# Performance work log

Hardware: AMD Instinct MI355X
Metric: run time of the kernel (lower is better)

The kernel has to match this reference:

```python
import jax, jax.numpy as jnp
import numpy as np

N_NODES = 100000
N_EDGES = 3200000
D_FEAT = 256
HIDDEN = 16


def setup_inputs() -> dict:
    key = jax.random.key(0)
    k1, k2, k3, k4 = jax.random.split(key, 4)
    x = jax.random.normal(k1, (N_NODES, D_FEAT), dtype=jnp.float32)
    edge_index = jax.random.randint(k2, (2, N_EDGES), 0, N_NODES, dtype=jnp.int64)
    # GCNConv linear weight (Glorot-ish scale) and bias
    W = jax.random.normal(k3, (D_FEAT, HIDDEN), dtype=jnp.float32) / np.sqrt(D_FEAT)
    b_conv = jnp.zeros((HIDDEN,), dtype=jnp.float32)
    W_fc = jax.random.normal(k4, (HIDDEN, 1), dtype=jnp.float32) / np.sqrt(HIDDEN)
    b_fc = jnp.zeros((1,), dtype=jnp.float32)
    return {"x": x, "edge_index": edge_index, "W": W, "b_conv": b_conv,
            "W_fc": W_fc, "b_fc": b_fc}


def reference(x, edge_index, W, b_conv, W_fc, b_fc):
    N = x.shape[0]
    # --- GCNConv: add self-loops, symmetric normalization, transform, scatter-add ---
    loop = jnp.arange(N, dtype=edge_index.dtype)
    src = jnp.concatenate([edge_index[0], loop])  # message sources (x_j)
    dst = jnp.concatenate([edge_index[1], loop])  # aggregation targets
    # degree of target nodes (edge weights = 1, self-loops included)
    deg = jax.ops.segment_sum(jnp.ones_like(dst, dtype=x.dtype), dst, num_segments=N)
    dinv = jnp.where(deg > 0, jax.lax.rsqrt(deg), 0.0)
    norm = dinv[src] * dinv[dst]  # [E+N]
    h = x @ W                       # [N, hidden] transform before propagation
    msg = h[src] * norm[:, None]    # gather + scale
    agg = jax.ops.segment_sum(msg, dst, num_segments=N)  # scatter-add
    out = agg + b_conv
    return out @ W_fc + b_fc
```

## Files before the change

kernel.cpp:

```cpp
#include <hip/hip_runtime.h>

#define DF 256
#define HID 16
#define WB 512
#define PBITS 8
#define PMAX 512

__global__ void __launch_bounds__(512)
hist_sval_kernel(const float* __restrict__ x, const int* __restrict__ dst,
                 const float* __restrict__ Wm, const float* __restrict__ W_fc,
                 unsigned* __restrict__ cntT, float* __restrict__ sv,
                 int N, int E, int P, int Epw) {
    __shared__ unsigned h[PMAX];
    for (int i = threadIdx.x; i < P; i += blockDim.x) h[i] = 0u;
    __syncthreads();
    const int w = blockIdx.x;
    const size_t e0 = (size_t)w * Epw;
    int m = (int)((size_t)E > e0 ? (size_t)E - e0 : 0);
    if (m > Epw) m = Epw;
    for (int i = threadIdx.x; i < m; i += blockDim.x)
        atomicAdd(&h[((unsigned)dst[e0 + i]) >> PBITS], 1u);
    __syncthreads();
    for (int p = threadIdx.x; p < P; p += blockDim.x)
        cntT[(size_t)p * WB + w] = h[p];

    const int lane = threadIdx.x & 63, wid = threadIdx.x >> 6;
    float a0 = 0.f, a1 = 0.f, a2 = 0.f, a3 = 0.f;
    const float* wrow = Wm + (size_t)(lane * 4) * HID;
#pragma unroll
    for (int j = 0; j < HID; ++j) {
        float f = W_fc[j];
        a0 += wrow[j] * f;
        a1 += wrow[HID + j] * f;
        a2 += wrow[2 * HID + j] * f;
        a3 += wrow[3 * HID + j] * f;
    }
    for (int row = blockIdx.x * 8 + wid; row < N; row += WB * 8) {
        float4 xv = reinterpret_cast<const float4*>(x + (size_t)row * DF)[lane];
        float acc = xv.x * a0 + xv.y * a1 + xv.z * a2 + xv.w * a3;
#pragma unroll
        for (int off = 32; off > 0; off >>= 1) acc += __shfl_xor(acc, off, 64);
        if (lane == 0) sv[row] = acc;
    }
}

__global__ void __launch_bounds__(WB)
rowscan_kernel(unsigned* __restrict__ cntT, unsigned* __restrict__ rowTotal) {
    __shared__ unsigned wsum[8];
    const int p = blockIdx.x, t = threadIdx.x;
    const int lane = t & 63, wid = t >> 6;
    unsigned v = cntT[(size_t)p * WB + t];
    unsigned xi = v;
#pragma unroll
    for (int off = 1; off < 64; off <<= 1) {
        unsigned u = __shfl_up(xi, off, 64);
        if (lane >= off) xi += u;
    }
    if (lane == 63) wsum[wid] = xi;
    __syncthreads();
    if (t < 8) {
        unsigned u = wsum[t];
#pragma unroll
        for (int off = 1; off < 8; off <<= 1) {
            unsigned uu = __shfl_up(u, off, 64);
            if (t >= off) u += uu;
        }
        wsum[t] = u;
    }
    __syncthreads();
    unsigned base = wid ? wsum[wid - 1] : 0u;
    cntT[(size_t)p * WB + t] = xi - v + base;
    if (t == 0) rowTotal[p] = wsum[7];
}

__global__ void __launch_bounds__(PMAX)
partscan_kernel(const unsigned* __restrict__ rowTotal, unsigned* __restrict__ partBase,
                int P, int E) {
    __shared__ unsigned wsum[8];
    const int t = threadIdx.x, lane = t & 63, wid = t >> 6;
    unsigned v = (t < P) ? rowTotal[t] : 0u;
    unsigned xi = v;
#pragma unroll
    for (int off = 1; off < 64; off <<= 1) {
        unsigned u = __shfl_up(xi, off, 64);
        if (lane >= off) xi += u;
    }
    if (lane == 63) wsum[wid] = xi;
    __syncthreads();
    if (t < 8) {
        unsigned u = wsum[t];
#pragma unroll
        for (int off = 1; off < 8; off <<= 1) {
            unsigned uu = __shfl_up(u, off, 64);
            if (t >= off) u += uu;
        }
        wsum[t] = u;
    }
    __syncthreads();
    unsigned base = wid ? wsum[wid - 1] : 0u;
    if (t < P) partBase[t] = xi - v + base;
    if (t == 0) partBase[P] = (unsigned)E;
}

__global__ void __launch_bounds__(512)
binscatter_kernel(const int* __restrict__ src, const int* __restrict__ dst,
                  const unsigned* __restrict__ cntT, const unsigned* __restrict__ partBase,
                  unsigned* __restrict__ sorted, int P, int E, int Epw) {
    __shared__ unsigned cur[PMAX];
    const int w = blockIdx.x;
    for (int p = threadIdx.x; p < P; p += blockDim.x)
        cur[p] = partBase[p] + cntT[(size_t)p * WB + w];
    __syncthreads();
    const size_t e0 = (size_t)w * Epw;
    int m = (int)((size_t)E > e0 ? (size_t)E - e0 : 0);
    if (m > Epw) m = Epw;
    for (int i = threadIdx.x; i < m; i += blockDim.x) {
        unsigned s = (unsigned)src[e0 + i];
        unsigned d = (unsigned)dst[e0 + i];
        unsigned slot = atomicAdd(&cur[d >> PBITS], 1u);
        sorted[slot] = (s << PBITS) | (d & 255u);
    }
}

__global__ void __launch_bounds__(1024)
degfin_kernel(const unsigned* __restrict__ sorted, const unsigned* __restrict__ partBase,
              const float* __restrict__ sv, float* __restrict__ dinv,
              float* __restrict__ tval, int N) {
    __shared__ unsigned dc[256];
    const int p = blockIdx.x;
    if (threadIdx.x < 256) dc[threadIdx.x] = 0u;
    __syncthreads();
    const unsigned b0 = partBase[p], b1 = partBase[p + 1];
    for (unsigned j = b0 + threadIdx.x; j < b1; j += blockDim.x)
        atomicAdd(&dc[sorted[j] & 255u], 1u);
    __syncthreads();
    if (threadIdx.x < 256) {
        int i = (p << PBITS) + (int)threadIdx.x;
        if (i < N) {
            float deg = 1.0f + (float)dc[threadIdx.x];
            float di = rsqrtf(deg);
            dinv[i] = di;
            tval[i] = sv[i] * di;
        }
    }
}

__global__ void __launch_bounds__(1024)
reduce_kernel(const unsigned* __restrict__ sorted, const unsigned* __restrict__ partBase,
              const float* __restrict__ tval, const float* __restrict__ dinv,
              const float* __restrict__ sv, const float* __restrict__ b_conv,
              const float* __restrict__ W_fc, const float* __restrict__ b_fc,
              float* __restrict__ out, int N) {
    __shared__ float facc[256];
    const int p = blockIdx.x;
    if (threadIdx.x < 256) facc[threadIdx.x] = 0.f;
    __syncthreads();
    const unsigned b0 = partBase[p], b1 = partBase[p + 1];
    for (unsigned j = b0 + threadIdx.x; j < b1; j += blockDim.x) {
        unsigned e = sorted[j];
        atomicAdd(&facc[e & 255u], tval[e >> PBITS]);
    }
    __syncthreads();
    if (threadIdx.x < 256) {
        int i = (p << PBITS) + (int)threadIdx.x;
        if (i < N) {
            float c = 0.f;
#pragma unroll
            for (int j = 0; j < HID; ++j) c += b_conv[j] * W_fc[j];
            float di = dinv[i];
            out[i] = sv[i] * di * di + c + b_fc[0] + di * facc[threadIdx.x];
        }
    }
}

__global__ void fb_sval(const float* __restrict__ x, const float* __restrict__ Wm,
                        const float* __restrict__ W_fc, float* __restrict__ sv, int N) {
    __shared__ float wl[DF];
    int k = threadIdx.x;
    float a = 0.f;
#pragma unroll
    for (int j = 0; j < HID; ++j) a += Wm[k * HID + j] * W_fc[j];
    wl[k] = a;
    __syncthreads();
    int lane = threadIdx.x & 63, wid = threadIdx.x >> 6;
    float4 wv = reinterpret_cast<const float4*>(wl)[lane];
    for (int row = blockIdx.x * 4 + wid; row < N; row += gridDim.x * 4) {
        float4 xv = reinterpret_cast<const float4*>(x + (size_t)row * DF)[lane];
        float acc = xv.x * wv.x + xv.y * wv.y + xv.z * wv.z + xv.w * wv.w;
#pragma unroll
        for (int off = 32; off > 0; off >>= 1) acc += __shfl_xor(acc, off, 64);
        if (lane == 0) sv[row] = acc;
    }
}
__global__ void fb_count(const int* __restrict__ dst, unsigned* __restrict__ cnt, int E) {
    int stride = gridDim.x * blockDim.x;
    for (int e = blockIdx.x * blockDim.x + threadIdx.x; e < E; e += stride)
        atomicAdd(&cnt[dst[e]], 1u);
}
__global__ void fb_node(const unsigned* __restrict__ cnt, const float* __restrict__ sv,
                        const float* __restrict__ b_conv, const float* __restrict__ W_fc,
                        const float* __restrict__ b_fc, float* __restrict__ dinv,
                        float* __restrict__ tval, float* __restrict__ out, int N) {
    int i = blockIdx.x * blockDim.x + threadIdx.x;
    if (i < N) {
        float c = 0.f;
#pragma unroll
        for (int j = 0; j < HID; ++j) c += b_conv[j] * W_fc[j];
        float deg = 1.0f + (float)cnt[i];
        float di = rsqrtf(deg);
        float s = sv[i];
        dinv[i] = di; tval[i] = s * di;
        out[i] = s / deg + c + b_fc[0];
    }
}
__global__ void fb_scatter(const int* __restrict__ src, const int* __restrict__ dst,
                           const float* __restrict__ tval, const float* __restrict__ dinv,
                           float* __restrict__ out, int E) {
    int stride = gridDim.x * blockDim.x;
    for (int e = blockIdx.x * blockDim.x + threadIdx.x; e < E; e += stride) {
        int si = src[e], di = dst[e];
        atomicAdd(&out[di], tval[si] * dinv[di]);
    }
}

extern "C" void kernel_launch(void* const* d_in, const int* in_sizes, int n_in,
                              void* d_out, int out_size, void* d_ws, size_t ws_size,
                              hipStream_t stream) {
    const float* x      = (const float*)d_in[0];
    const int*   ei     = (const int*)d_in[1];
    const float* Wm     = (const float*)d_in[2];
    const float* b_conv = (const float*)d_in[3];
    const float* W_fc   = (const float*)d_in[4];
    const float* b_fc   = (const float*)d_in[5];
    float* out = (float*)d_out;

    const int N = in_sizes[0] / DF;
    const int E = in_sizes[1] / 2;
    const int* src = ei;
    const int* dst = ei + E;

    const int P   = (N + 255) >> PBITS;
    const int Epw = (E + WB - 1) / WB;

    char* ws = (char*)d_ws;
    float* sv   = (float*)ws;
    float* dinv = sv + N;
    float* tval = dinv + N;
    unsigned* cntT     = (unsigned*)(tval + N);
    unsigned* rowTotal = cntT + (size_t)P * WB;
    unsigned* partBase = rowTotal + 512;
    unsigned* sorted   = partBase + 520;

    const size_t need = ((size_t)3 * N + (size_t)P * WB + 512 + 520 + (size_t)E) * 4;

    if (P >= 1 && P <= PMAX && N <= (1 << 23) && ws_size >= need) {
        hist_sval_kernel<<<WB, 512, 0, stream>>>(x, dst, Wm, W_fc, cntT, sv, N, E, P, Epw);
        rowscan_kernel<<<P, WB, 0, stream>>>(cntT, rowTotal);
        partscan_kernel<<<1, PMAX, 0, stream>>>(rowTotal, partBase, P, E);
        binscatter_kernel<<<WB, 512, 0, stream>>>(src, dst, cntT, partBase, sorted, P, E, Epw);
        degfin_kernel<<<P, 1024, 0, stream>>>(sorted, partBase, sv, dinv, tval, N);
        reduce_kernel<<<P, 1024, 0, stream>>>(sorted, partBase, tval, dinv, sv,
                                              b_conv, W_fc, b_fc, out, N);
    } else {
        unsigned* fcnt = (unsigned*)(tval + N);
        hipMemsetAsync(fcnt, 0, (size_t)N * 4, stream);
        fb_sval<<<2048, 256, 0, stream>>>(x, Wm, W_fc, sv, N);
        fb_count<<<2048, 256, 0, stream>>>(dst, fcnt, E);
        fb_node<<<(N + 255) / 256, 256, 0, stream>>>(fcnt, sv, b_conv, W_fc, b_fc, dinv, tval, out, N);
        fb_scatter<<<2048, 256, 0, stream>>>(src, dst, tval, dinv, out, E);
    }
}
```

Before: 90.96 us.

## Move x-projection into degree kernel, double histogram blocks, unroll edge loops

The x·(W·W_fc) row projection moves out of the histogram kernel and into the per-partition degree kernel, which now computes its 256 rows locally and drops the sv buffer. The final output reuses tval (sv·dinv), which removes a global read. The histogram gets 1024 blocks of 256 threads, and the histogram, scatter, degree and reduce edge loops are unrolled by four to keep more loads in flight. The trade-off is that the 100 MB x read now happens inside a kernel with only P blocks (~391), which may limit bandwidth, and the larger cntT makes the row scans heavier.

```diff
diff --git a/kernel.cpp b/kernel.cpp
--- a/kernel.cpp
+++ b/kernel.cpp
@@ -2,53 +2,37 @@
 
 #define DF 256
 #define HID 16
-#define WB 512
+#define WB 1024
 #define PBITS 8
 #define PMAX 512
 
-__global__ void __launch_bounds__(512)
-hist_sval_kernel(const float* __restrict__ x, const int* __restrict__ dst,
-                 const float* __restrict__ Wm, const float* __restrict__ W_fc,
-                 unsigned* __restrict__ cntT, float* __restrict__ sv,
-                 int N, int E, int P, int Epw) {
+__global__ void __launch_bounds__(256)
+hist_kernel(const int* __restrict__ dst, unsigned* __restrict__ cntT, int P, int E, int Epw) {
     __shared__ unsigned h[PMAX];
-    for (int i = threadIdx.x; i < P; i += blockDim.x) h[i] = 0u;
+    for (int i = threadIdx.x; i < P; i += 256) h[i] = 0u;
     __syncthreads();
     const int w = blockIdx.x;
     const size_t e0 = (size_t)w * Epw;
-    int m = (int)((size_t)E > e0 ? (size_t)E - e0 : 0);
-    if (m > Epw) m = Epw;
-    for (int i = threadIdx.x; i < m; i += blockDim.x)
-        atomicAdd(&h[((unsigned)dst[e0 + i]) >> PBITS], 1u);
-    __syncthreads();
-    for (int p = threadIdx.x; p < P; p += blockDim.x)
-        cntT[(size_t)p * WB + w] = h[p];
-
-    const int lane = threadIdx.x & 63, wid = threadIdx.x >> 6;
-    float a0 = 0.f, a1 = 0.f, a2 = 0.f, a3 = 0.f;
-    const float* wrow = Wm + (size_t)(lane * 4) * HID;
-#pragma unroll
-    for (int j = 0; j < HID; ++j) {
-        float f = W_fc[j];
-        a0 += wrow[j] * f;
-        a1 += wrow[HID + j] * f;
-        a2 += wrow[2 * HID + j] * f;
-        a3 += wrow[3 * HID + j] * f;
-    }
-    for (int row = blockIdx.x * 8 + wid; row < N; row += WB * 8) {
-        float4 xv = reinterpret_cast<const float4*>(x + (size_t)row * DF)[lane];
-        float acc = xv.x * a0 + xv.y * a1 + xv.z * a2 + xv.w * a3;
-#pragma unroll
-        for (int off = 32; off > 0; off >>= 1) acc += __shfl_xor(acc, off, 64);
-        if (lane == 0) sv[row] = acc;
-    }
-}
-
-__global__ void __launch_bounds__(WB)
+    long rem = (long)E - (long)e0;
+    int m = rem < 0 ? 0 : (rem > Epw ? Epw : (int)rem);
+    int i = threadIdx.x;
+    for (; i + 768 < m; i += 1024) {
+        unsigned d0 = (unsigned)dst[e0 + i];
+        unsigned d1 = (unsigned)dst[e0 + i + 256];
+        unsigned d2 = (unsigned)dst[e0 + i + 512];
+        unsigned d3 = (unsigned)dst[e0 + i + 768];
+        atomicAdd(&h[d0 >> PBITS], 1u); atomicAdd(&h[d1 >> PBITS], 1u);
+        atomicAdd(&h[d2 >> PBITS], 1u); atomicAdd(&h[d3 >> PBITS], 1u);
+    }
+    for (; i < m; i += 256) atomicAdd(&h[((unsigned)dst[e0 + i]) >> PBITS], 1u);
+    __syncthreads();
+    for (int p = threadIdx.x; p < P; p += 256) cntT[(size_t)p * WB + w] = h[p];
+}
+
+__global__ void __launch_bounds__(1024)
 rowscan_kernel(unsigned* __restrict__ cntT, unsigned* __restrict__ rowTotal) {
-    __shared__ unsigned wsum[8];
-    const int p = blockIdx.x, t = threadIdx.x;
-    const int lane = t & 63, wid = t >> 6;
+    __shared__ unsigned wsum[16];
+    const int p = blockIdx.x, t = threadIdx.x, lane = t & 63, wv = t >> 6;
     unsigned v = cntT[(size_t)p * WB + t];
     unsigned xi = v;
 #pragma unroll
@@ -56,7 +40,36 @@
         unsigned u = __shfl_up(xi, off, 64);
         if (lane >= off) xi += u;
     }
-    if (lane == 63) wsum[wid] = xi;
+    if (lane == 63) wsum[wv] = xi;
+    __syncthreads();
+    if (t < 16) {
+        unsigned u = wsum[t];
+#pragma unroll
+        for (int off = 1; off < 16; off <<= 1) {
+            unsigned uu = __shfl_up(u, off, 64);
+            if (t >= off) u += uu;
+        }
+        wsum[t] = u;
+    }
+    __syncthreads();
+    unsigned base = wv ? wsum[wv - 1] : 0u;
+    cntT[(size_t)p * WB + t] = xi - v + base;
+    if (t == 1023) rowTotal[p] = xi + base;
+}
+
+__global__ void __launch_bounds__(512)
+partscan_kernel(const unsigned* __restrict__ rowTotal, unsigned* __restrict__ partBase,
+                int P, int E) {
+    __shared__ unsigned wsum[8];
+    const int t = threadIdx.x, lane = t & 63, wv = t >> 6;
+    unsigned v = (t < P) ? rowTotal[t] : 0u;
+    unsigned xi = v;
+#pragma unroll
+    for (int off = 1; off < 64; off <<= 1) {
+        unsigned u = __shfl_up(xi, off, 64);
+        if (lane >= off) xi += u;
+    }
+    if (lane == 63) wsum[wv] = xi;
     __syncthreads();
     if (t < 8) {
         unsigned u = wsum[t];
@@ -68,36 +81,7 @@
         wsum[t] = u;
     }
     __syncthreads();
-    unsigned base = wid ? wsum[wid - 1] : 0u;
-    cntT[(size_t)p * WB + t] = xi - v + base;
-    if (t == 0) rowTotal[p] = wsum[7];
-}
-
-__global__ void __launch_bounds__(PMAX)
-partscan_kernel(const unsigned* __restrict__ rowTotal, unsigned* __restrict__ partBase,
-                int P, int E) {
-    __shared__ unsigned wsum[8];
-    const int t = threadIdx.x, lane = t & 63, wid = t >> 6;
-    unsigned v = (t < P) ? rowTotal[t] : 0u;
-    unsigned xi = v;
-#pragma unroll
-    for (int off = 1; off < 64; off <<= 1) {
-        unsigned u = __shfl_up(xi, off, 64);
-        if (lane >= off) xi += u;
-    }
-    if (lane == 63) wsum[wid] = xi;
-    __syncthreads();
-    if (t < 8) {
-        unsigned u = wsum[t];
-#pragma unroll
-        for (int off = 1; off < 8; off <<= 1) {
-            unsigned uu = __shfl_up(u, off, 64);
-            if (t >= off) u += uu;
-        }
-        wsum[t] = u;
-    }
-    __syncthreads();
-    unsigned base = wid ? wsum[wid - 1] : 0u;
+    unsigned base = wv ? wsum[wv - 1] : 0u;
     if (t < P) partBase[t] = xi - v + base;
     if (t == 0) partBase[P] = (unsigned)E;
 }
@@ -108,39 +92,92 @@
                   unsigned* __restrict__ sorted, int P, int E, int Epw) {
     __shared__ unsigned cur[PMAX];
     const int w = blockIdx.x;
-    for (int p = threadIdx.x; p < P; p += blockDim.x)
+    for (int p = threadIdx.x; p < P; p += 512)
         cur[p] = partBase[p] + cntT[(size_t)p * WB + w];
     __syncthreads();
     const size_t e0 = (size_t)w * Epw;
-    int m = (int)((size_t)E > e0 ? (size_t)E - e0 : 0);
-    if (m > Epw) m = Epw;
-    for (int i = threadIdx.x; i < m; i += blockDim.x) {
-        unsigned s = (unsigned)src[e0 + i];
-        unsigned d = (unsigned)dst[e0 + i];
+    long rem = (long)E - (long)e0;
+    int m = rem < 0 ? 0 : (rem > Epw ? Epw : (int)rem);
+    int i = threadIdx.x;
+    for (; i + 1536 < m; i += 2048) {
+        unsigned s0 = (unsigned)src[e0 + i],        d0 = (unsigned)dst[e0 + i];
+        unsigned s1 = (unsigned)src[e0 + i + 512],  d1 = (unsigned)dst[e0 + i + 512];
+        unsigned s2 = (unsigned)src[e0 + i + 1024], d2 = (unsigned)dst[e0 + i + 1024];
+        unsigned s3 = (unsigned)src[e0 + i + 1536], d3 = (unsigned)dst[e0 + i + 1536];
+        unsigned t0 = atomicAdd(&cur[d0 >> PBITS], 1u);
+        unsigned t1 = atomicAdd(&cur[d1 >> PBITS], 1u);
+        unsigned t2 = atomicAdd(&cur[d2 >> PBITS], 1u);
+        unsigned t3 = atomicAdd(&cur[d3 >> PBITS], 1u);
+        sorted[t0] = (s0 << PBITS) | (d0 & 255u);
+        sorted[t1] = (s1 << PBITS) | (d1 & 255u);
+        sorted[t2] = (s2 << PBITS) | (d2 & 255u);
+        sorted[t3] = (s3 << PBITS) | (d3 & 255u);
+    }
+    for (; i < m; i += 512) {
+        unsigned s = (unsigned)src[e0 + i], d = (unsigned)dst[e0 + i];
         unsigned slot = atomicAdd(&cur[d >> PBITS], 1u);
         sorted[slot] = (s << PBITS) | (d & 255u);
     }
 }
 
 __global__ void __launch_bounds__(1024)
-degfin_kernel(const unsigned* __restrict__ sorted, const unsigned* __restrict__ partBase,
-              const float* __restrict__ sv, float* __restrict__ dinv,
-              float* __restrict__ tval, int N) {
+degfin_sval_kernel(const float* __restrict__ x, const unsigned* __restrict__ sorted,
+                   const unsigned* __restrict__ partBase, const float* __restrict__ Wm,
+                   const float* __restrict__ W_fc, float* __restrict__ dinv,
+                   float* __restrict__ tval, int N) {
     __shared__ unsigned dc[256];
-    const int p = blockIdx.x;
-    if (threadIdx.x < 256) dc[threadIdx.x] = 0u;
+    __shared__ float sly[256];
+    const int p = blockIdx.x, t = threadIdx.x;
+    if (t < 256) dc[t] = 0u;
     __syncthreads();
     const unsigned b0 = partBase[p], b1 = partBase[p + 1];
-    for (unsigned j = b0 + threadIdx.x; j < b1; j += blockDim.x)
-        atomicAdd(&dc[sorted[j] & 255u], 1u);
-    __syncthreads();
-    if (threadIdx.x < 256) {
-        int i = (p << PBITS) + (int)threadIdx.x;
+    unsigned j = b0 + t;
+    for (; j + 3072 < b1; j += 4096) {
+        unsigned e0 = sorted[j], e1 = sorted[j + 1024], e2 = sorted[j + 2048], e3 = sorted[j + 3072];
+        atomicAdd(&dc[e0 & 255u], 1u); atomicAdd(&dc[e1 & 255u], 1u);
+        atomicAdd(&dc[e2 & 255u], 1u); atomicAdd(&dc[e3 & 255u], 1u);
+    }
+    for (; j < b1; j += 1024) atomicAdd(&dc[sorted[j] & 255u], 1u);
+    {
+        const int lane = t & 63, wv = t >> 6;
+        float a0 = 0.f, a1 = 0.f, a2 = 0.f, a3 = 0.f;
+        const float* wrow = Wm + (size_t)(lane * 4) * HID;
+#pragma unroll
+        for (int k = 0; k < HID; ++k) {
+            float f = W_fc[k];
+            a0 += wrow[k] * f;
+            a1 += wrow[HID + k] * f;
+            a2 += wrow[2 * HID + k] * f;
+            a3 += wrow[3 * HID + k] * f;
+        }
+        for (int k = 0; k < 8; ++k) {
+            int ra = wv + 16 * k, rb = ra + 128;
+            int ia = (p << PBITS) + ra, ib = (p << PBITS) + rb;
+            float sa = 0.f, sb = 0.f;
+            if (ia < N) {
+                float4 xa = reinterpret_cast<const float4*>(x + (size_t)ia * DF)[lane];
+                sa = xa.x * a0 + xa.y * a1 + xa.z * a2 + xa.w * a3;
+            }
+            if (ib < N) {
+                float4 xb = reinterpret_cast<const float4*>(x + (size_t)ib * DF)[lane];
+                sb = xb.x * a0 + xb.y * a1 + xb.z * a2 + xb.w * a3;
+            }
+#pragma unroll
+            for (int off = 32; off > 0; off >>= 1) {
+                sa += __shfl_xor(sa, off, 64);
+                sb += __shfl_xor(sb, off, 64);
+            }
+            if (lane == 0) { sly[ra] = sa; sly[rb] = sb; }
+        }
+    }
+    __syncthreads();
+    if (t < 256) {
+        int i = (p << PBITS) + t;
         if (i < N) {
-            float deg = 1.0f + (float)dc[threadIdx.x];
+            float deg = 1.0f + (float)dc[t];
             float di = rsqrtf(deg);
             dinv[i] = di;
-            tval[i] = sv[i] * di;
+            tval[i] = sly[t] * di;
         }
     }
 }
@@ -148,27 +185,34 @@
 __global__ void __launch_bounds__(1024)
 reduce_kernel(const unsigned* __restrict__ sorted, const unsigned* __restrict__ partBase,
               const float* __restrict__ tval, const float* __restrict__ dinv,
-              const float* __restrict__ sv, const float* __restrict__ b_conv,
-              const float* __restrict__ W_fc, const float* __restrict__ b_fc,
-              float* __restrict__ out, int N) {
+              const float* __restrict__ b_conv, const float* __restrict__ W_fc,
+              const float* __restrict__ b_fc, float* __restrict__ out, int N) {
     __shared__ float facc[256];
-    const int p = blockIdx.x;
-    if (threadIdx.x < 256) facc[threadIdx.x] = 0.f;
+    const int p = blockIdx.x, t = threadIdx.x;
+    if (t < 256) facc[t] = 0.f;
     __syncthreads();
     const unsigned b0 = partBase[p], b1 = partBase[p + 1];
-    for (unsigned j = b0 + threadIdx.x; j < b1; j += blockDim.x) {
+    unsigned j = b0 + t;
+    for (; j + 3072 < b1; j += 4096) {
+        unsigned e0 = sorted[j], e1 = sorted[j + 1024], e2 = sorted[j + 2048], e3 = sorted[j + 3072];
+        float v0 = tval[e0 >> PBITS], v1 = tval[e1 >> PBITS];
+        float v2 = tval[e2 >> PBITS], v3 = tval[e3 >> PBITS];
+        atomicAdd(&facc[e0 & 255u], v0); atomicAdd(&facc[e1 & 255u], v1);
+        atomicAdd(&facc[e2 & 255u], v2); atomicAdd(&facc[e3 & 255u], v3);
+    }
+    for (; j < b1; j += 1024) {
         unsigned e = sorted[j];
         atomicAdd(&facc[e & 255u], tval[e >> PBITS]);
     }
     __syncthreads();
-    if (threadIdx.x < 256) {
-        int i = (p << PBITS) + (int)threadIdx.x;
+    if (t < 256) {
+        int i = (p << PBITS) + t;
         if (i < N) {
             float c = 0.f;
 #pragma unroll
-            for (int j = 0; j < HID; ++j) c += b_conv[j] * W_fc[j];
+            for (int k = 0; k < HID; ++k) c += b_conv[k] * W_fc[k];
             float di = dinv[i];
-            out[i] = sv[i] * di * di + c + b_fc[0] + di * facc[threadIdx.x];
+            out[i] = di * (tval[i] + facc[t]) + c + b_fc[0];
         }
     }
 }
@@ -243,26 +287,26 @@
     const int Epw = (E + WB - 1) / WB;
 
     char* ws = (char*)d_ws;
-    float* sv   = (float*)ws;
-    float* dinv = sv + N;
+    float* dinv = (float*)ws;
     float* tval = dinv + N;
     unsigned* cntT     = (unsigned*)(tval + N);
     unsigned* rowTotal = cntT + (size_t)P * WB;
     unsigned* partBase = rowTotal + 512;
     unsigned* sorted   = partBase + 520;
 
-    const size_t need = ((size_t)3 * N + (size_t)P * WB + 512 + 520 + (size_t)E) * 4;
+    const size_t need = ((size_t)2 * N + (size_t)P * WB + 512 + 520 + (size_t)E) * 4;
 
     if (P >= 1 && P <= PMAX && N <= (1 << 23) && ws_size >= need) {
-        hist_sval_kernel<<<WB, 512, 0, stream>>>(x, dst, Wm, W_fc, cntT, sv, N, E, P, Epw);
-        rowscan_kernel<<<P, WB, 0, stream>>>(cntT, rowTotal);
-        partscan_kernel<<<1, PMAX, 0, stream>>>(rowTotal, partBase, P, E);
+        hist_kernel<<<WB, 256, 0, stream>>>(dst, cntT, P, E, Epw);
+        rowscan_kernel<<<P, 1024, 0, stream>>>(cntT, rowTotal);
+        partscan_kernel<<<1, 512, 0, stream>>>(rowTotal, partBase, P, E);
         binscatter_kernel<<<WB, 512, 0, stream>>>(src, dst, cntT, partBase, sorted, P, E, Epw);
-        degfin_kernel<<<P, 1024, 0, stream>>>(sorted, partBase, sv, dinv, tval, N);
-        reduce_kernel<<<P, 1024, 0, stream>>>(sorted, partBase, tval, dinv, sv,
+        degfin_sval_kernel<<<P, 1024, 0, stream>>>(x, sorted, partBase, Wm, W_fc, dinv, tval, N);
+        reduce_kernel<<<P, 1024, 0, stream>>>(sorted, partBase, tval, dinv,
                                               b_conv, W_fc, b_fc, out, N);
     } else {
-        unsigned* fcnt = (unsigned*)(tval + N);
+        float* sv = tval + N;
+        unsigned* fcnt = (unsigned*)(sv + N);
         hipMemsetAsync(fcnt, 0, (size_t)N * 4, stream);
         fb_sval<<<2048, 256, 0, stream>>>(x, Wm, W_fc, sv, N);
         fb_count<<<2048, 256, 0, stream>>>(dst, fcnt, E);
```

New measurement: 101.0 us. 1.11x slower.
